# Performance work log

Measured on AMD Instinct MI355X. Metric: run time of the kernel, lower is better.

Reference implementation:

```python
import jax, jax.numpy as jnp
import numpy as np
import math

H, D_MODEL, D_C, D_ROPE = 16, 2048, 512, 64
D_HEAD = D_MODEL // H  # 128
D_QK = D_HEAD + D_ROPE  # 192


def precompute_freqs_cis(d_rope, seq_len, base=10000.0):
    # standard RoPE frequencies over pairs -> (seq_len, d_rope//2)
    inv_freq = 1.0 / (base ** (jnp.arange(0, d_rope, 2, dtype=jnp.float32) / d_rope))
    t = jnp.arange(seq_len, dtype=jnp.float32)
    ang = jnp.outer(t, inv_freq)
    return jnp.cos(ang), jnp.sin(ang)


def apply_rotary_emb(x, cos, sin):
    # x: (..., T, d_rope); cos/sin broadcastable (..., T, d_rope//2); interleaved pairs
    x1 = x[..., 0::2]
    x2 = x[..., 1::2]
    r1 = x1 * cos - x2 * sin
    r2 = x1 * sin + x2 * cos
    return jnp.stack([r1, r2], axis=-1).reshape(x.shape)


def setup_inputs() -> dict:
    key = jax.random.key(0)
    ks = jax.random.split(key, 10)
    B, T = 2, 2048
    s = 0.02
    return {
        "query": jax.random.normal(ks[0], (B, T, D_MODEL), jnp.float32),
        "key": jax.random.normal(ks[1], (B, T, D_MODEL), jnp.float32),
        "value": jax.random.normal(ks[2], (B, T, D_MODEL), jnp.float32),
        # weights stored (in_dim, out_dim)
        "W_DKV": jax.random.normal(ks[3], (D_MODEL, D_C), jnp.float32) * s,
        "W_UK": jax.random.normal(ks[4], (D_C, H * D_HEAD), jnp.float32) * s,
        "W_UV": jax.random.normal(ks[5], (D_C, H * D_HEAD), jnp.float32) * s,
        "W_Q": jax.random.normal(ks[6], (D_MODEL, H * D_HEAD), jnp.float32) * s,
        "W_KR": jax.random.normal(ks[7], (D_MODEL, D_ROPE), jnp.float32) * s,
        "W_QR": jax.random.normal(ks[8], (D_MODEL, H * D_ROPE), jnp.float32) * s,
        "W_O": jax.random.normal(ks[9], (H * D_HEAD, D_MODEL), jnp.float32) * s,
    }


def reference(query, key, value, W_DKV, W_UK, W_UV, W_Q, W_KR, W_QR, W_O):
    B, T_q, _ = query.shape
    T_k = key.shape[1]
    # low-rank latent KV compression
    c_kv = key @ W_DKV                                   # (B, Tk, d_c)
    k_nope = (c_kv @ W_UK).reshape(B, T_k, H, D_HEAD).transpose(0, 2, 1, 3)  # bhkd
    v = (c_kv @ W_UV).reshape(B, T_k, H, D_HEAD).transpose(0, 2, 1, 3)       # bhkd
    q_nope = (query @ W_Q).reshape(B, T_q, H, D_HEAD).transpose(0, 2, 1, 3)  # bhqd
    # decoupled RoPE subspace
    k_rope_in = (key @ W_KR)[:, None, :, :]              # (B,1,Tk,d_rope) shared across heads
    q_rope_in = (query @ W_QR).reshape(B, T_q, H, D_ROPE).transpose(0, 2, 1, 3)
    cos_q, sin_q = precompute_freqs_cis(D_ROPE, T_q)
    cos_k, sin_k = precompute_freqs_cis(D_ROPE, T_k)
    q_rope = apply_rotary_emb(q_rope_in, cos_q[None, None], sin_q[None, None])
    k_rope = apply_rotary_emb(k_rope_in, cos_k[None, None], sin_k[None, None])
    k_rope = jnp.broadcast_to(k_rope, (B, H, T_k, D_ROPE))
    # concat content + rope parts
    q = jnp.concatenate([q_nope, q_rope], axis=-1)       # (B,H,Tq,d_qk)
    k = jnp.concatenate([k_nope, k_rope], axis=-1)       # (B,H,Tk,d_qk)
    scores = jnp.einsum('bhqd,bhkd->bhqk', q, k) / math.sqrt(D_QK)
    p_attn = jax.nn.softmax(scores, axis=-1)             # dropout is identity (eval/p=0)
    x = jnp.einsum('bhqk,bhkd->bhqd', p_attn, v)
    x = x.transpose(0, 2, 1, 3).reshape(B, T_q, H * D_HEAD)
    output = x @ W_O
    return output, p_attn
```

## Files before the change

### kernel.cpp

```cpp
#include <hip/hip_runtime.h>
#include <hip/hip_bf16.h>
#include <math.h>

constexpr int B_   = 2;
constexpr int T_   = 2048;
constexpr int DM   = 2048;
constexpr int H_   = 16;
constexpr int DH   = 128;
constexpr int DC   = 512;
constexpr int DR   = 64;
constexpr int DQK  = DH + DR;
constexpr int BT   = B_ * T_;
constexpr int ZBH  = B_ * H_;

typedef __bf16 bf16x8 __attribute__((ext_vector_type(8)));
typedef float  f32x4  __attribute__((ext_vector_type(4)));
typedef unsigned int u32x2 __attribute__((ext_vector_type(2)));
typedef unsigned short u16x4 __attribute__((ext_vector_type(4)));

__device__ __forceinline__ unsigned pk2(float a, float b) {
  __hip_bfloat162 t = __float22bfloat162_rn(make_float2(a, b));
  return *reinterpret_cast<unsigned*>(&t);
}
__device__ __forceinline__ unsigned short bfbits(float v) {
  __hip_bfloat16 t = __float2bfloat16(v);
  return *reinterpret_cast<unsigned short*>(&t);
}

#define WAITVM(N)   asm volatile("s_waitcnt vmcnt(" #N ")" ::: "memory")
#define BARSB() do { __builtin_amdgcn_s_barrier(); __builtin_amdgcn_sched_barrier(0); } while (0)
#define AS1 __attribute__((address_space(1)))
#define AS3 __attribute__((address_space(3)))

__global__ __launch_bounds__(256)
void prep(const float* __restrict__ query, const float* __restrict__ key,
          const float* __restrict__ W_Q, const float* __restrict__ W_QR,
          const float* __restrict__ W_DKV, const float* __restrict__ W_KR,
          const float* __restrict__ W_UK, const float* __restrict__ W_UV,
          const float* __restrict__ W_O,
          __hip_bfloat16* __restrict__ qB, __hip_bfloat16* __restrict__ kB,
          __hip_bfloat16* __restrict__ Wtqall, __hip_bfloat16* __restrict__ Wtkall,
          __hip_bfloat16* __restrict__ Wtkvup, __hip_bfloat16* __restrict__ WtO,
          float* __restrict__ ctab, float* __restrict__ stab) {
  __shared__ float tile[32][33];
  const int blk = blockIdx.x;
  const int tid = threadIdx.x;

  if (blk < 4096) {
    const float* src = (blk < 2048) ? query : key;
    __hip_bfloat16* dst = (blk < 2048) ? qB : kB;
    const long base = (long)(blk & 2047) * 4096;
    #pragma unroll
    for (int c = 0; c < 4; ++c) {
      const long off = base + c * 1024 + tid * 4;
      float4 f = *(const float4*)(src + off);
      u16x4 pk;
      pk[0] = bfbits(f.x); pk[1] = bfbits(f.y); pk[2] = bfbits(f.z); pk[3] = bfbits(f.w);
      *(u16x4*)(dst + off) = pk;
    }
    return;
  }

  int b = blk - 4096;
  const float* W = nullptr; __hip_bfloat16* Wt = nullptr; int K = 2048, N = 2048;
  if (b < 4096)               { W = W_Q;   Wt = Wtqall; }
  else if ((b -= 4096) < 2048){ W = W_QR;  Wt = Wtqall + (size_t)2048 * 2048; N = 1024; }
  else if ((b -= 2048) < 1024){ W = W_DKV; Wt = Wtkall; N = 512; }
  else if ((b -= 1024) < 128) { W = W_KR;  Wt = Wtkall + (size_t)512 * 2048; N = 64; }
  else if ((b -= 128) < 1024) { W = W_UK;  Wt = Wtkvup; K = 512; }
  else if ((b -= 1024) < 1024){ W = W_UV;  Wt = Wtkvup + (size_t)2048 * 512; K = 512; }
  else if ((b -= 1024) < 4096){ W = W_O;   Wt = WtO; }
  else if ((b -= 4096) < 192) {
    float4 z = {0.f, 0.f, 0.f, 0.f};
    *(float4*)((char*)(Wtkall + (size_t)(576 + b) * 2048) + tid * 16) = z;
    return;
  }
  else {
    b -= 192;
    const int i = b * 256 + tid;
    const int t = i >> 5, j = i & 31;
    double inv = pow(10000.0, -(double)j / 32.0);
    double ang = (double)t * inv;
    ctab[i] = (float)cos(ang);
    stab[i] = (float)sin(ang);
    return;
  }
  const int nx = N >> 5;
  const int n0 = (b % nx) << 5, k0 = (b / nx) << 5;
  const int tx = tid & 31, ty = tid >> 5;
  for (int i = ty; i < 32; i += 8)
    tile[i][tx] = W[(long)(k0 + i) * N + n0 + tx];
  __syncthreads();
  for (int i = ty; i < 32; i += 8)
    Wt[(long)(n0 + i) * K + k0 + tx] = __float2bfloat16(tile[tx][i]);
}

template <int MODE>
__device__ __forceinline__
void gemm4w_core(const __hip_bfloat16* __restrict__ A, const __hip_bfloat16* __restrict__ Bt,
                 void* __restrict__ C0, void* __restrict__ C1,
                 int N, int K, int lda,
                 const float* __restrict__ ctab, const float* __restrict__ stab,
                 int bid, int nwg, char* lds) {
  const int gnx = N >> 8;
  const int cpx = nwg >> 3;
  const int swz = (bid & 7) * cpx + (bid >> 3);
  const int n0 = (swz % gnx) << 8;
  const int m0 = (swz / gnx) << 7;

  const int tid  = threadIdx.x;
  const int wc   = tid >> 6;
  const int lane = tid & 63;
  const int rr   = lane & 15;
  const int kq   = lane >> 4;

  const int cs16 = (((tid & 3) ^ ((tid >> 3) & 3)) << 4);
  const int srow = tid >> 2;

  auto stage = [&](int buf, int k0) {
    char* base = lds + buf * 24576;
    #pragma unroll
    for (int c = 0; c < 2; ++c) {
      const char* src = (const char*)A + (((long)(m0 + c * 64 + srow)) * lda + k0) * 2 + cs16;
      __builtin_amdgcn_global_load_lds((const AS1 void*)src,
          (AS3 void*)(base + c * 4096 + tid * 16), 16, 0, 0);
    }
    #pragma unroll
    for (int c = 0; c < 4; ++c) {
      const char* src = (const char*)Bt + (((long)(n0 + c * 64 + srow)) * K + k0) * 2 + cs16;
      __builtin_amdgcn_global_load_lds((const AS1 void*)src,
          (AS3 void*)(base + 8192 + c * 4096 + tid * 16), 16, 0, 0);
    }
  };

  const int g16 = ((kq ^ ((rr >> 1) & 3)) << 4);
  const int aoff0 = rr * 64 + g16;
  const int boff0 = 8192 + (wc * 64 + rr) * 64 + g16;

  f32x4 acc[8][4] = {};

  auto phase = [&](int buf) {
    char* base = lds + buf * 24576;
    bf16x8 a[8], b[4];
    #pragma unroll
    for (int mf = 0; mf < 8; ++mf) a[mf] = *(const bf16x8*)(base + aoff0 + mf * 1024);
    #pragma unroll
    for (int nf = 0; nf < 4; ++nf) b[nf] = *(const bf16x8*)(base + boff0 + nf * 1024);
    __builtin_amdgcn_s_setprio(1);
    #pragma unroll
    for (int mf = 0; mf < 8; ++mf)
      #pragma unroll
      for (int nf = 0; nf < 4; ++nf)
        acc[mf][nf] = __builtin_amdgcn_mfma_f32_16x16x32_bf16(a[mf], b[nf], acc[mf][nf], 0, 0, 0);
    __builtin_amdgcn_s_setprio(0);
  };

  const int NT = K >> 5;
  stage(0, 0); stage(1, 32);
  int cur = 0;
  for (int t = 0; t < NT; ++t) {
    if (t + 1 < NT) WAITVM(6); else WAITVM(0);
    BARSB();
    if (t + 2 < NT) {
      const int b2 = (cur + 2 >= 3) ? cur - 1 : cur + 2;
      stage(b2, (t + 2) << 5);
    }
    phase(cur);
    cur = (cur + 1 >= 3) ? 0 : cur + 1;
  }

  #pragma unroll
  for (int mf = 0; mf < 8; ++mf) {
    #pragma unroll
    for (int nf = 0; nf < 4; ++nf) {
      const int col = n0 + wc * 64 + nf * 16 + rr;
      const int rbase = m0 + mf * 16 + kq * 4;
      if constexpr (MODE == 1) {
        float* C = (float*)C0;
        #pragma unroll
        for (int j = 0; j < 4; ++j)
          __builtin_nontemporal_store(acc[mf][nf][j], &C[(long)(rbase + j) * N + col]);
      } else if constexpr (MODE == 2) {
        __hip_bfloat16* qall = (__hip_bfloat16*)C0;
        if (col < 2048) {
          #pragma unroll
          for (int j = 0; j < 4; ++j)
            qall[(long)(rbase + j) * 3072 + col] = __float2bfloat16(acc[mf][nf][j]);
        } else {
          const int dr = (col - 2048) & 63;
          const int jj = dr >> 1;
          #pragma unroll
          for (int j = 0; j < 4; ++j) {
            const int row = rbase + j;
            const int t = row & (T_ - 1);
            const float c = ctab[t * 32 + jj], s = stab[t * 32 + jj];
            const float v  = acc[mf][nf][j];
            const float pv = __shfl_xor(v, 1);
            const float res = (dr & 1) ? (pv * s + v * c) : (v * c - pv * s);
            qall[(long)row * 3072 + col] = __float2bfloat16(res);
          }
        }
      } else if constexpr (MODE == 3) {
        __hip_bfloat16* ckv = (__hip_bfloat16*)C0;
        __hip_bfloat16* krp = (__hip_bfloat16*)C1;
        if (col < 512) {
          #pragma unroll
          for (int j = 0; j < 4; ++j)
            ckv[(long)(rbase + j) * 512 + col] = __float2bfloat16(acc[mf][nf][j]);
        } else if (col < 576) {
          const int dr = col - 512;
          const int jj = dr >> 1;
          #pragma unroll
          for (int j = 0; j < 4; ++j) {
            const int row = rbase + j;
            const int t = row & (T_ - 1);
            const float c = ctab[t * 32 + jj], s = stab[t * 32 + jj];
            const float v  = acc[mf][nf][j];
            const float pv = __shfl_xor(v, 1);
            const float res = (dr & 1) ? (pv * s + v * c) : (v * c - pv * s);
            krp[(long)row * 64 + dr] = __float2bfloat16(res);
          }
        }
      } else if constexpr (MODE == 4) {
        __hip_bfloat16* knope = (__hip_bfloat16*)C0;
        __hip_bfloat16* vT    = (__hip_bfloat16*)C1;
        if (col < 2048) {
          #pragma unroll
          for (int j = 0; j < 4; ++j)
            knope[(long)(rbase + j) * 2048 + col] = __float2bfloat16(acc[mf][nf][j]);
        } else {
          const int h = (col - 2048) >> 7, d = (col - 2048) & 127;
          const int z = (rbase >> 11) * 16 + h;
          const int t0 = rbase & (T_ - 1);
          u16x4 pk;
          #pragma unroll
          for (int j = 0; j < 4; ++j) pk[j] = bfbits(acc[mf][nf][j]);
          *(u16x4*)((__hip_bfloat16*)vT + ((long)z * DH + d) * T_ + t0) = pk;
        }
      }
    }
  }
}

template <int MODE>
__global__ __launch_bounds__(256, 2)
void gemm_4w(const __hip_bfloat16* __restrict__ A, const __hip_bfloat16* __restrict__ Bt,
             void* __restrict__ C0, void* __restrict__ C1,
             int M, int N, int K, int lda,
             const float* __restrict__ ctab, const float* __restrict__ stab) {
  __shared__ __align__(16) char lds[73728];
  gemm4w_core<MODE>(A, Bt, C0, C1, N, K, lda, ctab, stab,
                    blockIdx.x, (M >> 7) * (N >> 8), lds);
}

__global__ __launch_bounds__(256, 2)
void proj_qk(const __hip_bfloat16* __restrict__ qB, const __hip_bfloat16* __restrict__ kB,
             const __hip_bfloat16* __restrict__ Wtqall, const __hip_bfloat16* __restrict__ Wtkall,
             __hip_bfloat16* __restrict__ q_all, __hip_bfloat16* __restrict__ ckv,
             __hip_bfloat16* __restrict__ kroper,
             const float* __restrict__ ctab, const float* __restrict__ stab) {
  __shared__ __align__(16) char lds[73728];
  if (blockIdx.x < 384)
    gemm4w_core<2>(qB, Wtqall, q_all, nullptr, 3072, 2048, 2048, ctab, stab,
                   blockIdx.x, 384, lds);
  else
    gemm4w_core<3>(kB, Wtkall, ckv, kroper, 768, 2048, 2048, ctab, stab,
                   blockIdx.x - 384, 96, lds);
}

__global__ __launch_bounds__(512)
void fused_attn(const __hip_bfloat16* __restrict__ q_all,
                const __hip_bfloat16* __restrict__ knope,
                const __hip_bfloat16* __restrict__ kroper,
                const __hip_bfloat16* __restrict__ vTg,
                float* __restrict__ patt,
                __hip_bfloat16* __restrict__ xplain) {
  constexpr int KT = 64;
  constexpr int NKT = T_ / KT;
  const int bid = blockIdx.x;
  const int swz = (bid & 7) * 64 + (bid >> 3);
  const int z  = swz >> 4;
  const int q0 = (swz & 15) << 7;
  const int b  = z >> 4, h = z & 15;
  const int tid  = threadIdx.x;
  const int wv   = tid >> 6;
  const int lane = tid & 63;
  const int rr   = lane & 15;
  const int kq   = lane >> 4;
  const float scl = 0.0721687836487032f;

  __shared__ __align__(16) char smem[98304];
  char* const lP = smem + 81920;

  const long qrow = (long)(b * T_) + q0 + wv * 16 + rr;
  const __hip_bfloat16* qn = q_all + qrow * 3072 + h * 128;
  const __hip_bfloat16* qr = q_all + qrow * 3072 + 2048 + h * 64;
  bf16x8 qa[6];
  #pragma unroll
  for (int kc = 0; kc < 4; ++kc) qa[kc] = *(const bf16x8*)(qn + kc * 32 + kq * 8);
  #pragma unroll
  for (int kc = 0; kc < 2; ++kc) qa[4 + kc] = *(const bf16x8*)(qr + kc * 32 + kq * 8);

  auto stage_k = [&](char* dst, int kt0) {
    #pragma unroll
    for (int it = 0; it < 3; ++it) {
      const int off = it * 8192 + wv * 1024;
      const int lb  = off + lane * 16;
      const int row = lb / 384, cb = lb % 384;
      const int scb = cb ^ ((row & 7) << 4);
      const long trow = (long)(b * T_) + kt0 + row;
      const char* src = (scb < 256)
          ? (const char*)knope + trow * 4096 + h * 256 + scb
          : (const char*)kroper + trow * 128 + (scb - 256);
      __builtin_amdgcn_global_load_lds((const AS1 void*)src,
          (AS3 void*)(dst + off), 16, 0, 0);
    }
  };
  auto stage_v = [&](char* dst, int kt0) {
    #pragma unroll
    for (int it = 0; it < 2; ++it) {
      const int off = it * 8192 + wv * 1024;
      const int lb  = off + lane * 16;
      const int row = lb >> 7, cb = lb & 127;
      const int scb = cb ^ ((row & 7) << 4);
      const char* src = (const char*)vTg + ((long)(z * DH + row) * T_ + kt0) * 2 + scb;
      __builtin_amdgcn_global_load_lds((const AS1 void*)src,
          (AS3 void*)(dst + off), 16, 0, 0);
    }
  };

  auto qkt = [&](const char* kb0, f32x4 (&sacc)[4]) {
    __builtin_amdgcn_s_setprio(1);
    #pragma unroll
    for (int kc = 0; kc < 6; ++kc) {
      #pragma unroll
      for (int n = 0; n < 4; ++n) {
        const int krow = n * 16 + rr;
        bf16x8 kb = *(const bf16x8*)(kb0 + krow * 384 +
                                     ((kc * 64 + kq * 16) ^ ((krow & 7) << 4)));
        sacc[n] = __builtin_amdgcn_mfma_f32_16x16x32_bf16(kb, qa[kc], sacc[n], 0, 0, 0);
      }
    }
    __builtin_amdgcn_s_setprio(0);
  };

  float srun = 0.f;

  stage_k(smem, 0);
  stage_k(smem + 24576, KT);
  for (int kt = 0; kt < NKT; ++kt) {
    if (kt + 2 < NKT)      { stage_k(smem + ((kt + 2) & 3) * 24576, (kt + 2) * KT); WAITVM(6); }
    else if (kt + 2 == NKT) WAITVM(3);
    else                    WAITVM(0);
    BARSB();
    f32x4 sacc[4] = {};
    qkt(smem + (kt & 3) * 24576, sacc);
    float ts = 0.f;
    #pragma unroll
    for (int n = 0; n < 4; ++n)
      #pragma unroll
      for (int r = 0; r < 4; ++r) ts += __expf(sacc[n][r] * scl);
    ts += __shfl_xor(ts, 16);
    ts += __shfl_xor(ts, 32);
    srun += ts;
  }
  const float pis = 1.f / srun;

  stage_k(smem, 0);
  stage_v(smem + 49152, 0);
  BARSB();

  f32x4 oacc[8] = {};
  const int prow = wv * 16 + rr;
  int cur = 0;
  for (int kt = 0; kt < NKT; ++kt) {
    if (kt == 0) WAITVM(0); else WAITVM(4);
    BARSB();
    if (kt + 1 < NKT) {
      stage_k(smem + (cur ? 0 : 24576), (kt + 1) * KT);
      stage_v(smem + 49152 + (cur ? 0 : 16384), (kt + 1) * KT);
    }
    const char* lK = smem + (cur ? 24576 : 0);
    const char* lV = smem + 49152 + (cur ? 16384 : 0);
    f32x4 sacc[4] = {};
    qkt(lK, sacc);
    const int kt0 = kt * KT;
    #pragma unroll
    for (int n = 0; n < 4; ++n) {
      f32x4 pv;
      #pragma unroll
      for (int r = 0; r < 4; ++r) pv[r] = __expf(sacc[n][r] * scl) * pis;
      __builtin_nontemporal_store(pv,
          (f32x4*)(patt + ((long)z * T_ + q0 + prow) * T_ + kt0 + n * 16 + kq * 4));
      u32x2 pw; pw[0] = pk2(pv[0], pv[1]); pw[1] = pk2(pv[2], pv[3]);
      *(u32x2*)(lP + prow * 128 + ((n * 32 + kq * 8) ^ ((prow & 7) << 4))) = pw;
    }
    bf16x8 pa[2];
    #pragma unroll
    for (int kc = 0; kc < 2; ++kc)
      pa[kc] = *(const bf16x8*)(lP + prow * 128 + ((kc * 64 + kq * 16) ^ ((prow & 7) << 4)));
    __builtin_amdgcn_s_setprio(1);
    #pragma unroll
    for (int kc = 0; kc < 2; ++kc) {
      #pragma unroll
      for (int n = 0; n < 8; ++n) {
        const int vrow = n * 16 + rr;
        bf16x8 vb = *(const bf16x8*)(lV + vrow * 128 + ((kc * 64 + kq * 16) ^ ((vrow & 7) << 4)));
        oacc[n] = __builtin_amdgcn_mfma_f32_16x16x32_bf16(pa[kc], vb, oacc[n], 0, 0, 0);
      }
    }
    __builtin_amdgcn_s_setprio(0);
    cur ^= 1;
  }

  #pragma unroll
  for (int n = 0; n < 8; ++n) {
    #pragma unroll
    for (int r = 0; r < 4; ++r) {
      const int q = q0 + wv * 16 + kq * 4 + r;
      xplain[((long)(b * T_ + q)) * DM + h * DH + n * 16 + rr] = __float2bfloat16(oacc[n][r]);
    }
  }
}

extern "C" void kernel_launch(void* const* d_in, const int* in_sizes, int n_in,
                              void* d_out, int out_size, void* d_ws, size_t ws_size,
                              hipStream_t stream) {
  const float* query = (const float*)d_in[0];
  const float* key   = (const float*)d_in[1];
  const float* W_DKV = (const float*)d_in[3];
  const float* W_UK  = (const float*)d_in[4];
  const float* W_UV  = (const float*)d_in[5];
  const float* W_Q   = (const float*)d_in[6];
  const float* W_KR  = (const float*)d_in[7];
  const float* W_QR  = (const float*)d_in[8];
  const float* W_O   = (const float*)d_in[9];

  float* out  = (float*)d_out;
  float* patt = out + (long)BT * DM;

  char* w = (char*)d_ws;
  auto alloc = [&](size_t bytes) { char* p = w; w += (bytes + 255) & ~(size_t)255; return p; };
  __hip_bfloat16* qB     = (__hip_bfloat16*)alloc((size_t)BT * DM * 2);
  __hip_bfloat16* kB     = (__hip_bfloat16*)alloc((size_t)BT * DM * 2);
  __hip_bfloat16* Wtqall = (__hip_bfloat16*)alloc((size_t)3072 * DM * 2);
  __hip_bfloat16* Wtkall = (__hip_bfloat16*)alloc((size_t)768 * DM * 2);
  __hip_bfloat16* Wtkvup = (__hip_bfloat16*)alloc((size_t)4096 * DC * 2);
  __hip_bfloat16* WtO    = (__hip_bfloat16*)alloc((size_t)DM * DM * 2);
  __hip_bfloat16* q_all  = (__hip_bfloat16*)alloc((size_t)BT * 3072 * 2);
  __hip_bfloat16* ckv    = (__hip_bfloat16*)alloc((size_t)BT * 512 * 2);
  __hip_bfloat16* kroper = (__hip_bfloat16*)alloc((size_t)BT * 64 * 2);
  __hip_bfloat16* knope  = (__hip_bfloat16*)alloc((size_t)BT * 2048 * 2);
  __hip_bfloat16* vT     = (__hip_bfloat16*)alloc((size_t)ZBH * DH * T_ * 2);
  __hip_bfloat16* xplain = (__hip_bfloat16*)alloc((size_t)BT * DM * 2);
  float*          ctab   = (float*)alloc((size_t)T_ * 32 * 4);
  float*          stab   = (float*)alloc((size_t)T_ * 32 * 4);

  prep<<<dim3(17984), 256, 0, stream>>>(
      query, key, W_Q, W_QR, W_DKV, W_KR, W_UK, W_UV, W_O,
      qB, kB, Wtqall, Wtkall, Wtkvup, WtO, ctab, stab);

  proj_qk<<<dim3(480), 256, 0, stream>>>(
      qB, kB, Wtqall, Wtkall, q_all, ckv, kroper, ctab, stab);

  gemm_4w<4><<<dim3(512), 256, 0, stream>>>(
      ckv, Wtkvup, knope, vT, BT, 4096, DC, 512, nullptr, nullptr);

  fused_attn<<<dim3(512), 512, 0, stream>>>(
      q_all, knope, kroper, vT, patt, xplain);

  gemm_4w<1><<<dim3(256), 256, 0, stream>>>(
      xplain, WtO, out, nullptr, BT, DM, DM, DM, nullptr, nullptr);
}
```

Baseline: 398.7 us.

## Double query rows per attention block to reuse K/V tiles across two row groups

```diff
diff --git a/kernel.cpp b/kernel.cpp
--- a/kernel.cpp
+++ b/kernel.cpp
@@ -278,9 +278,9 @@
   constexpr int KT = 64;
   constexpr int NKT = T_ / KT;
   const int bid = blockIdx.x;
-  const int swz = (bid & 7) * 64 + (bid >> 3);
-  const int z  = swz >> 4;
-  const int q0 = (swz & 15) << 7;
+  const int swz = (bid & 7) * 32 + (bid >> 3);
+  const int z  = swz >> 3;
+  const int q0 = (swz & 7) << 8;
   const int b  = z >> 4, h = z & 15;
   const int tid  = threadIdx.x;
   const int wv   = tid >> 6;
@@ -289,17 +289,25 @@
   const int kq   = lane >> 4;
   const float scl = 0.0721687836487032f;
 
-  __shared__ __align__(16) char smem[98304];
+  __shared__ __align__(16) char smem[114688];
   char* const lP = smem + 81920;
 
-  const long qrow = (long)(b * T_) + q0 + wv * 16 + rr;
-  const __hip_bfloat16* qn = q_all + qrow * 3072 + h * 128;
-  const __hip_bfloat16* qr = q_all + qrow * 3072 + 2048 + h * 64;
-  bf16x8 qa[6];
-  #pragma unroll
-  for (int kc = 0; kc < 4; ++kc) qa[kc] = *(const bf16x8*)(qn + kc * 32 + kq * 8);
-  #pragma unroll
-  for (int kc = 0; kc < 2; ++kc) qa[4 + kc] = *(const bf16x8*)(qr + kc * 32 + kq * 8);
+  const long qrow0 = (long)(b * T_) + q0 + wv * 32 + rr;
+  bf16x8 qa0[6], qa1[6];
+  {
+    const __hip_bfloat16* qn = q_all + qrow0 * 3072 + h * 128;
+    const __hip_bfloat16* qr = q_all + qrow0 * 3072 + 2048 + h * 64;
+    #pragma unroll
+    for (int kc = 0; kc < 4; ++kc) qa0[kc] = *(const bf16x8*)(qn + kc * 32 + kq * 8);
+    #pragma unroll
+    for (int kc = 0; kc < 2; ++kc) qa0[4 + kc] = *(const bf16x8*)(qr + kc * 32 + kq * 8);
+    const __hip_bfloat16* qn1 = qn + 16 * 3072;
+    const __hip_bfloat16* qr1 = qr + 16 * 3072;
+    #pragma unroll
+    for (int kc = 0; kc < 4; ++kc) qa1[kc] = *(const bf16x8*)(qn1 + kc * 32 + kq * 8);
+    #pragma unroll
+    for (int kc = 0; kc < 2; ++kc) qa1[4 + kc] = *(const bf16x8*)(qr1 + kc * 32 + kq * 8);
+  }
 
   auto stage_k = [&](char* dst, int kt0) {
     #pragma unroll
@@ -329,7 +337,7 @@
     }
   };
 
-  auto qkt = [&](const char* kb0, f32x4 (&sacc)[4]) {
+  auto qkt = [&](const char* kb0, f32x4 (&s0)[4], f32x4 (&s1)[4]) {
     __builtin_amdgcn_s_setprio(1);
     #pragma unroll
     for (int kc = 0; kc < 6; ++kc) {
@@ -338,13 +346,14 @@
         const int krow = n * 16 + rr;
         bf16x8 kb = *(const bf16x8*)(kb0 + krow * 384 +
                                      ((kc * 64 + kq * 16) ^ ((krow & 7) << 4)));
-        sacc[n] = __builtin_amdgcn_mfma_f32_16x16x32_bf16(kb, qa[kc], sacc[n], 0, 0, 0);
+        s0[n] = __builtin_amdgcn_mfma_f32_16x16x32_bf16(kb, qa0[kc], s0[n], 0, 0, 0);
+        s1[n] = __builtin_amdgcn_mfma_f32_16x16x32_bf16(kb, qa1[kc], s1[n], 0, 0, 0);
       }
     }
     __builtin_amdgcn_s_setprio(0);
   };
 
-  float srun = 0.f;
+  float srun0 = 0.f, srun1 = 0.f;
 
   stage_k(smem, 0);
   stage_k(smem + 24576, KT);
@@ -353,28 +362,29 @@
     else if (kt + 2 == NKT) WAITVM(3);
     else                    WAITVM(0);
     BARSB();
-    f32x4 sacc[4] = {};
-    qkt(smem + (kt & 3) * 24576, sacc);
-    float ts = 0.f;
+    f32x4 s0[4] = {}, s1[4] = {};
+    qkt(smem + (kt & 3) * 24576, s0, s1);
+    float t0 = 0.f, t1 = 0.f;
     #pragma unroll
     for (int n = 0; n < 4; ++n)
       #pragma unroll
-      for (int r = 0; r < 4; ++r) ts += __expf(sacc[n][r] * scl);
-    ts += __shfl_xor(ts, 16);
-    ts += __shfl_xor(ts, 32);
-    srun += ts;
-  }
-  const float pis = 1.f / srun;
+      for (int r = 0; r < 4; ++r) { t0 += __expf(s0[n][r] * scl); t1 += __expf(s1[n][r] * scl); }
+    t0 += __shfl_xor(t0, 16); t0 += __shfl_xor(t0, 32);
+    t1 += __shfl_xor(t1, 16); t1 += __shfl_xor(t1, 32);
+    srun0 += t0; srun1 += t1;
+  }
+  const float pis0 = 1.f / srun0;
+  const float pis1 = 1.f / srun1;
 
   stage_k(smem, 0);
   stage_v(smem + 49152, 0);
   BARSB();
 
-  f32x4 oacc[8] = {};
-  const int prow = wv * 16 + rr;
+  f32x4 o0[8] = {}, o1[8] = {};
+  const int prow = wv * 32 + rr;
   int cur = 0;
   for (int kt = 0; kt < NKT; ++kt) {
-    if (kt == 0) WAITVM(0); else WAITVM(4);
+    if (kt == 0) WAITVM(0); else WAITVM(8);
     BARSB();
     if (kt + 1 < NKT) {
       stage_k(smem + (cur ? 0 : 24576), (kt + 1) * KT);
@@ -382,23 +392,32 @@
     }
     const char* lK = smem + (cur ? 24576 : 0);
     const char* lV = smem + 49152 + (cur ? 16384 : 0);
-    f32x4 sacc[4] = {};
-    qkt(lK, sacc);
+    f32x4 s0[4] = {}, s1[4] = {};
+    qkt(lK, s0, s1);
     const int kt0 = kt * KT;
+    float* prow_g0 = patt + ((long)z * T_ + q0 + prow) * T_ + kt0;
+    float* prow_g1 = prow_g0 + 16 * (long)T_;
     #pragma unroll
     for (int n = 0; n < 4; ++n) {
-      f32x4 pv;
+      f32x4 pv0, pv1;
       #pragma unroll
-      for (int r = 0; r < 4; ++r) pv[r] = __expf(sacc[n][r] * scl) * pis;
-      __builtin_nontemporal_store(pv,
-          (f32x4*)(patt + ((long)z * T_ + q0 + prow) * T_ + kt0 + n * 16 + kq * 4));
-      u32x2 pw; pw[0] = pk2(pv[0], pv[1]); pw[1] = pk2(pv[2], pv[3]);
-      *(u32x2*)(lP + prow * 128 + ((n * 32 + kq * 8) ^ ((prow & 7) << 4))) = pw;
-    }
-    bf16x8 pa[2];
-    #pragma unroll
-    for (int kc = 0; kc < 2; ++kc)
-      pa[kc] = *(const bf16x8*)(lP + prow * 128 + ((kc * 64 + kq * 16) ^ ((prow & 7) << 4)));
+      for (int r = 0; r < 4; ++r) {
+        pv0[r] = __expf(s0[n][r] * scl) * pis0;
+        pv1[r] = __expf(s1[n][r] * scl) * pis1;
+      }
+      __builtin_nontemporal_store(pv0, (f32x4*)(prow_g0 + n * 16 + kq * 4));
+      __builtin_nontemporal_store(pv1, (f32x4*)(prow_g1 + n * 16 + kq * 4));
+      u32x2 pw0; pw0[0] = pk2(pv0[0], pv0[1]); pw0[1] = pk2(pv0[2], pv0[3]);
+      u32x2 pw1; pw1[0] = pk2(pv1[0], pv1[1]); pw1[1] = pk2(pv1[2], pv1[3]);
+      *(u32x2*)(lP + prow * 128 + ((n * 32 + kq * 8) ^ ((prow & 7) << 4))) = pw0;
+      *(u32x2*)(lP + (prow + 16) * 128 + ((n * 32 + kq * 8) ^ ((prow & 7) << 4))) = pw1;
+    }
+    bf16x8 pa0[2], pa1[2];
+    #pragma unroll
+    for (int kc = 0; kc < 2; ++kc) {
+      pa0[kc] = *(const bf16x8*)(lP + prow * 128 + ((kc * 64 + kq * 16) ^ ((prow & 7) << 4)));
+      pa1[kc] = *(const bf16x8*)(lP + (prow + 16) * 128 + ((kc * 64 + kq * 16) ^ ((prow & 7) << 4)));
+    }
     __builtin_amdgcn_s_setprio(1);
     #pragma unroll
     for (int kc = 0; kc < 2; ++kc) {
@@ -406,7 +425,8 @@
       for (int n = 0; n < 8; ++n) {
         const int vrow = n * 16 + rr;
         bf16x8 vb = *(const bf16x8*)(lV + vrow * 128 + ((kc * 64 + kq * 16) ^ ((vrow & 7) << 4)));
-        oacc[n] = __builtin_amdgcn_mfma_f32_16x16x32_bf16(pa[kc], vb, oacc[n], 0, 0, 0);
+        o0[n] = __builtin_amdgcn_mfma_f32_16x16x32_bf16(pa0[kc], vb, o0[n], 0, 0, 0);
+        o1[n] = __builtin_amdgcn_mfma_f32_16x16x32_bf16(pa1[kc], vb, o1[n], 0, 0, 0);
       }
     }
     __builtin_amdgcn_s_setprio(0);
@@ -417,8 +437,9 @@
   for (int n = 0; n < 8; ++n) {
     #pragma unroll
     for (int r = 0; r < 4; ++r) {
-      const int q = q0 + wv * 16 + kq * 4 + r;
-      xplain[((long)(b * T_ + q)) * DM + h * DH + n * 16 + rr] = __float2bfloat16(oacc[n][r]);
+      const int q = q0 + wv * 32 + kq * 4 + r;
+      xplain[((long)(b * T_ + q)) * DM + h * DH + n * 16 + rr] = __float2bfloat16(o0[n][r]);
+      xplain[((long)(b * T_ + q + 16)) * DM + h * DH + n * 16 + rr] = __float2bfloat16(o1[n][r]);
     }
   }
 }
@@ -466,7 +487,7 @@
   gemm_4w<4><<<dim3(512), 256, 0, stream>>>(
       ckv, Wtkvup, knope, vT, BT, 4096, DC, 512, nullptr, nullptr);
 
-  fused_attn<<<dim3(512), 512, 0, stream>>>(
+  fused_attn<<<dim3(256), 512, 0, stream>>>(
       q_all, knope, kroper, vT, patt, xplain);
 
   gemm_4w<1><<<dim3(256), 256, 0, stream>>>(
```

After: 421.5 us. 5.7% more time.
